# Kernel optimization log

Measured on AMD Instinct MI355X. Metric: run time of the kernel, lower is better.

## Reference

```python
import jax, jax.numpy as jnp
import numpy as np

ALPHA = 0.1   # margin alpha from __init__
K = 16        # retrieval fan-out
N_CLASSES = 100  # label range for mode computation (vals in [-1, N_CLASSES))


def setup_inputs() -> dict:
    key = jax.random.key(0)
    k1, k2, k3, k4 = jax.random.split(key, 4)
    queries = jax.random.normal(k1, (64, 512, 7, 7), dtype=jnp.float32)
    targets = jax.random.randint(k2, (64,), 0, 100, dtype=jnp.int32)
    m_keys = jax.random.normal(k3, (65536, 512), dtype=jnp.float32)
    m_keys = m_keys / jnp.linalg.norm(m_keys, axis=-1, keepdims=True)
    m_vals = jax.random.randint(k4, (65536,), 0, 100, dtype=jnp.int32)
    return {"queries": queries, "targets": targets, "m_keys": m_keys, "m_vals": m_vals}


def _forward(queries, targets, m_keys, m_vals):
    bs, c, h, w = queries.shape
    hw = h * w
    q = queries.reshape(bs, c, hw).transpose(0, 2, 1)            # [bs, hw, c]
    q = q / jnp.clip(jnp.linalg.norm(q, axis=-1, keepdims=True), 1e-12)  # F.normalize

    def per_item(qry, tgt):
        sims = qry @ m_keys.T                                    # [hw, M]
        # top-2 retrieval: fetched value = mode of nearest slot labels
        _, top2_idx = jax.lax.top_k(sims, 2)
        nearest_val = m_vals[top2_idx[:, 0]]                     # [hw]
        counts = jnp.zeros((N_CLASSES + 1,), jnp.int32).at[nearest_val + 1].add(1)
        fetched = jnp.argmax(counts).astype(jnp.int32) - 1
        # top-K retrieval for margin loss
        topk_sims, topk_idx = jax.lax.top_k(sims, K)             # [hw, K]
        topk_vals = m_vals[topk_idx]                             # [hw, K]
        # safety positive slot: first memory slot whose label == target
        hit = m_vals == tgt
        exists = jnp.any(hit)
        safety_idx = jnp.argmax(hit)
        safety_sim = sims[:, safety_idx]                         # [hw]
        ext_sims = jnp.concatenate([topk_sims, safety_sim[:, None]], axis=1)  # [hw, K+1]
        ext_vals = jnp.concatenate(
            [topk_vals, jnp.full((hw, 1), tgt, topk_vals.dtype)], axis=1)
        cmask = ext_vals == tgt
        pos = jnp.max(ext_sims * cmask, axis=-1)                 # topk(sims*mask, k=1)
        neg = jnp.max(ext_sims * (~cmask), axis=-1)
        loss_with = jnp.mean(jax.nn.relu(neg - pos + ALPHA))
        # branch where target class absent from memory
        neg_ns = jnp.max(topk_sims * (topk_vals != tgt), axis=-1)
        loss_ns = jnp.mean(jax.nn.relu(neg_ns + ALPHA))
        loss = jnp.where(exists, loss_with, loss_ns)
        return fetched, loss

    fetched_vals, losses = jax.vmap(per_item)(q, targets)
    return fetched_vals, jnp.sum(losses)


def reference(queries, targets, m_keys, m_vals):
    return _forward(queries, targets, m_keys, m_vals)
```

## Files before the change

### kernel.cpp

```cpp
#include <hip/hip_runtime.h>
#include <hip/hip_bf16.h>
#include <float.h>
#include <limits.h>

#define NROWS 3136
#define NROWS_PAD 3200
#define NKEYS 65536
#define KDIM 512
#define NITEMS 64
#define HW 49
#define TOPK 16
#define CAND 32
#define LANE_L 12
#define TKW 4
#define ALPHA_C 0.1f

typedef unsigned short u16;
typedef unsigned int u32;
typedef __attribute__((ext_vector_type(8))) short bfrag;
typedef __attribute__((ext_vector_type(4))) float f32x4;

__device__ inline u16 f2bf(float x) {
  u32 u = __float_as_uint(x);
  u32 r = u + 0x7fffu + ((u >> 16) & 1u);
  return (u16)(r >> 16);
}

__global__ __launch_bounds__(256) void prep_qnorm(const float* __restrict__ q,
        float* __restrict__ q_norm, u16* __restrict__ qbf) {
  int row = blockIdx.x;
  int t = threadIdx.x;
  if (row >= NROWS) {
    qbf[(size_t)row * KDIM + t] = 0;
    qbf[(size_t)row * KDIM + t + 256] = 0;
    return;
  }
  int b = row / HW, p = row % HW;
  const float* base = q + (size_t)b * KDIM * HW + p;
  float v0 = base[(size_t)t * HW];
  float v1 = base[(size_t)(t + 256) * HW];
  __shared__ float red[256];
  red[t] = v0 * v0 + v1 * v1;
  __syncthreads();
  for (int st = 128; st > 0; st >>= 1) {
    if (t < st) red[t] += red[t + st];
    __syncthreads();
  }
  float nrm = fmaxf(sqrtf(red[0]), 1e-12f);
  float w0 = v0 / nrm, w1 = v1 / nrm;
  q_norm[(size_t)row * KDIM + t] = w0;
  q_norm[(size_t)row * KDIM + t + 256] = w1;
  qbf[(size_t)row * KDIM + t] = f2bf(w0);
  qbf[(size_t)row * KDIM + t + 256] = f2bf(w1);
}

__global__ __launch_bounds__(256) void prep_keys(const float* __restrict__ mk, u16* __restrict__ kbf) {
  size_t i = ((size_t)blockIdx.x * 256 + threadIdx.x) * 8;
  float4 a = *(const float4*)(mk + i);
  float4 b = *(const float4*)(mk + i + 4);
  bfrag v;
  v[0] = (short)f2bf(a.x); v[1] = (short)f2bf(a.y);
  v[2] = (short)f2bf(a.z); v[3] = (short)f2bf(a.w);
  v[4] = (short)f2bf(b.x); v[5] = (short)f2bf(b.y);
  v[6] = (short)f2bf(b.z); v[7] = (short)f2bf(b.w);
  *(bfrag*)(kbf + i) = v;
}

__global__ void init_first(int* first_idx) {
  int t = threadIdx.x;
  if (t < 100) first_idx[t] = INT_MAX;
}
__global__ __launch_bounds__(256) void init_run(float* run_sim, int* run_idx) {
  int i = blockIdx.x * 256 + threadIdx.x;
  run_sim[i] = -FLT_MAX;
  run_idx[i] = INT_MAX;
}
__global__ __launch_bounds__(256) void scan_vals(const int* __restrict__ mvals, int* first_idx) {
  int i = blockIdx.x * 256 + threadIdx.x;
  atomicMin(&first_idx[mvals[i]], i);
}
__global__ void item_info(const int* __restrict__ targets, const int* __restrict__ first_idx,
                          int* item_saf, int* item_ex) {
  int b = threadIdx.x;
  int fi = first_idx[targets[b]];
  int ex = (fi != INT_MAX);
  item_ex[b] = ex;
  item_saf[b] = ex ? fi : 0;
}

__device__ inline void gload16(const void* g, void* l) {
  __builtin_amdgcn_global_load_lds((const __attribute__((address_space(1))) unsigned int*)g,
                                   (__attribute__((address_space(3))) unsigned int*)l, 16, 0, 0);
}

#define CT_LD 144

__global__ __launch_bounds__(256) void gemm_chunk(const u16* __restrict__ A, const u16* __restrict__ B,
        u16* __restrict__ C, int ldc) {
  __shared__ __align__(16) char lds[128 * CT_LD * 2];
  u16* As = (u16*)lds;
  u16* Bs = (u16*)(lds + 8192);
  u16* Ct = (u16*)lds;
  int tid = threadIdx.x;
  int lane = tid & 63, wv = tid >> 6;
  int wr = wv >> 1, wc = wv & 1;
  int mbase = blockIdx.x * 128;
  int nbase = blockIdx.y * 128;
  const u16* Ag = A + (size_t)mbase * KDIM;
  const u16* Bg = B + (size_t)nbase * KDIM;

  f32x4 acc[4][4];
  #pragma unroll
  for (int i = 0; i < 4; ++i)
    #pragma unroll
    for (int j = 0; j < 4; ++j)
      acc[i][j] = (f32x4){0.f, 0.f, 0.f, 0.f};

  int lrow = lane & 15;
  int k8 = (lane >> 4) * 8;

  for (int kk = 0; kk < KDIM; kk += 32) {
    #pragma unroll
    for (int s = 0; s < 2; ++s) {
      int ch = s * 256 + wv * 64 + lane;
      int r = ch >> 2, c = (ch & 3) * 8;
      gload16(Ag + (size_t)r * KDIM + kk + c, lds + (size_t)(s * 256 + wv * 64) * 16);
      gload16(Bg + (size_t)r * KDIM + kk + c, lds + 8192 + (size_t)(s * 256 + wv * 64) * 16);
    }
    __syncthreads();
    bfrag a[4], b[4];
    #pragma unroll
    for (int i = 0; i < 4; ++i) {
      a[i] = *(const bfrag*)&As[(wr * 64 + i * 16 + lrow) * 32 + k8];
      b[i] = *(const bfrag*)&Bs[(wc * 64 + i * 16 + lrow) * 32 + k8];
    }
    #pragma unroll
    for (int i = 0; i < 4; ++i)
      #pragma unroll
      for (int j = 0; j < 4; ++j)
        acc[i][j] = __builtin_amdgcn_mfma_f32_16x16x32_bf16(a[i], b[j], acc[i][j], 0, 0, 0);
    __syncthreads();
  }
  int r0l = wr * 64 + (lane >> 4) * 4;
  int c0l = wc * 64 + lrow;
  #pragma unroll
  for (int i = 0; i < 4; ++i)
    #pragma unroll
    for (int j = 0; j < 4; ++j)
      #pragma unroll
      for (int r = 0; r < 4; ++r)
        Ct[(r0l + i * 16 + r) * CT_LD + c0l + j * 16] = f2bf(acc[i][j][r]);
  __syncthreads();
  #pragma unroll
  for (int it = 0; it < 8; ++it) {
    int chnk = it * 256 + tid;
    int rr = chnk >> 4, cg = chnk & 15;
    uint4 v = *(const uint4*)&Ct[rr * CT_LD + cg * 8];
    *(uint4*)(C + (size_t)(mbase + rr) * ldc + nbase + cg * 8) = v;
  }
}

__device__ inline void ins_top(float (&s)[LANE_L], int (&ix)[LANE_L], float vv, int cidx) {
  if (vv > s[LANE_L - 1]) {
    #pragma unroll
    for (int k = LANE_L - 1; k >= 0; --k) {
      bool g  = vv > s[k];
      bool gp = (k > 0) && (vv > s[k - 1]);
      float ns = g ? (gp ? s[k - 1] : vv) : s[k];
      int   ni = g ? (gp ? ix[k - 1] : cidx) : ix[k];
      s[k] = ns; ix[k] = ni;
    }
  }
}

__global__ __launch_bounds__(256) void topk_update(const u16* __restrict__ C, int nk, int key_base,
        float* __restrict__ run_sim, int* __restrict__ run_idx) {
  int row = blockIdx.x;
  int tid = threadIdx.x, lane = tid & 63, wv = tid >> 6;
  int seg = nk >> 2;
  const u16* crow = C + (size_t)row * nk + (size_t)wv * seg;
  int ibase = key_base + wv * seg;

  float s[LANE_L]; int ix[LANE_L];
  #pragma unroll
  for (int k = 0; k < LANE_L; ++k) { s[k] = -FLT_MAX; ix[k] = INT_MAX; }

  int iters = seg >> 9;
  for (int t = 0; t < iters; ++t) {
    uint4 v = *(const uint4*)(crow + (size_t)t * 512 + lane * 8);
    int ib = ibase + t * 512 + lane * 8;
    ins_top(s, ix, __uint_as_float(v.x << 16), ib + 0);
    ins_top(s, ix, __uint_as_float(v.x & 0xffff0000u), ib + 1);
    ins_top(s, ix, __uint_as_float(v.y << 16), ib + 2);
    ins_top(s, ix, __uint_as_float(v.y & 0xffff0000u), ib + 3);
    ins_top(s, ix, __uint_as_float(v.z << 16), ib + 4);
    ins_top(s, ix, __uint_as_float(v.z & 0xffff0000u), ib + 5);
    ins_top(s, ix, __uint_as_float(v.w << 16), ib + 6);
    ins_top(s, ix, __uint_as_float(v.w & 0xffff0000u), ib + 7);
  }

  __shared__ float msim[TKW][CAND + 1]; __shared__ int midx[TKW][CAND + 1];
  __shared__ float rs[CAND + 1];        __shared__ int ri[CAND + 1];
  for (int r = 0; r < CAND; ++r) {
    float c = s[0]; int ci = ix[0];
    for (int off = 32; off > 0; off >>= 1) {
      float oc = __shfl_xor(c, off);
      int   oi = __shfl_xor(ci, off);
      if (oc > c || (oc == c && oi < ci)) { c = oc; ci = oi; }
    }
    if (lane == 0) { msim[wv][r] = c; midx[wv][r] = ci; }
    if (ci == ix[0]) {
      #pragma unroll
      for (int k = 0; k < LANE_L - 1; ++k) { s[k] = s[k + 1]; ix[k] = ix[k + 1]; }
      s[LANE_L - 1] = -FLT_MAX; ix[LANE_L - 1] = INT_MAX;
    }
  }
  if (lane == 0) { msim[wv][CAND] = -FLT_MAX; midx[wv][CAND] = INT_MAX; }
  if (tid < CAND) { rs[tid] = run_sim[row * CAND + tid]; ri[tid] = run_idx[row * CAND + tid]; }
  if (tid == 0)  { rs[CAND] = -FLT_MAX; ri[CAND] = INT_MAX; }
  __syncthreads();
  if (tid == 0) {
    int p0 = 0, p1 = 0, p2 = 0, p3 = 0, pr = 0;
    for (int o = 0; o < CAND; ++o) {
      float bs = rs[pr]; int bi = ri[pr]; int src = 4;
      float h; int hi;
      h = msim[0][p0]; hi = midx[0][p0]; if (h > bs || (h == bs && hi < bi)) { bs = h; bi = hi; src = 0; }
      h = msim[1][p1]; hi = midx[1][p1]; if (h > bs || (h == bs && hi < bi)) { bs = h; bi = hi; src = 1; }
      h = msim[2][p2]; hi = midx[2][p2]; if (h > bs || (h == bs && hi < bi)) { bs = h; bi = hi; src = 2; }
      h = msim[3][p3]; hi = midx[3][p3]; if (h > bs || (h == bs && hi < bi)) { bs = h; bi = hi; src = 3; }
      run_sim[row * CAND + o] = bs; run_idx[row * CAND + o] = bi;
      if (src == 0) ++p0; else if (src == 1) ++p1; else if (src == 2) ++p2;
      else if (src == 3) ++p3; else ++pr;
    }
  }
}

__global__ __launch_bounds__(64) void rescore(const float* __restrict__ q_norm, const float* __restrict__ mkeys,
        const int* __restrict__ mvals, const int* __restrict__ run_idx, const int* __restrict__ item_saf,
        float* __restrict__ t16_sim, int* __restrict__ t16_val, int* __restrict__ nearest_val,
        float* __restrict__ safety_sim) {
  int row = blockIdx.x, lane = threadIdx.x;
  int b = row / HW;
  const float* qr = q_norm + (size_t)row * KDIM;
  float4 q0 = *(const float4*)(qr + lane * 8);
  float4 q1 = *(const float4*)(qr + lane * 8 + 4);
  __shared__ float es[CAND]; __shared__ int ei[CAND];

  for (int c = 0; c < CAND; ++c) {
    int ki = run_idx[row * CAND + c];
    float p = -FLT_MAX;
    if (ki >= 0 && ki < NKEYS) {
      const float* kr = mkeys + (size_t)ki * KDIM;
      float4 k0 = *(const float4*)(kr + lane * 8);
      float4 k1 = *(const float4*)(kr + lane * 8 + 4);
      p = q0.x * k0.x + q0.y * k0.y + q0.z * k0.z + q0.w * k0.w
        + q1.x * k1.x + q1.y * k1.y + q1.z * k1.z + q1.w * k1.w;
      for (int off = 32; off > 0; off >>= 1) p += __shfl_xor(p, off);
    }
    if (lane == 0) { es[c] = p; ei[c] = (ki >= 0 && ki < NKEYS) ? ki : -1; }
  }
  {
    int ks = item_saf[b];
    const float* kr = mkeys + (size_t)ks * KDIM;
    float4 k0 = *(const float4*)(kr + lane * 8);
    float4 k1 = *(const float4*)(kr + lane * 8 + 4);
    float p = q0.x * k0.x + q0.y * k0.y + q0.z * k0.z + q0.w * k0.w
            + q1.x * k1.x + q1.y * k1.y + q1.z * k1.z + q1.w * k1.w;
    for (int off = 32; off > 0; off >>= 1) p += __shfl_xor(p, off);
    if (lane == 0) safety_sim[row] = p;
  }
  __syncthreads();
  if (lane == 0) {
    for (int r = 0; r < TOPK; ++r) {
      float bs = -FLT_MAX; int bi = INT_MAX, bc = -1;
      for (int c = 0; c < CAND; ++c) {
        if (ei[c] < 0) continue;
        if (es[c] > bs || (es[c] == bs && ei[c] < bi)) { bs = es[c]; bi = ei[c]; bc = c; }
      }
      if (bc < 0) { bs = 0.f; bi = 0; } else ei[bc] = -1;
      t16_sim[row * TOPK + r] = bs;
      t16_val[row * TOPK + r] = mvals[bi];
      if (r == 0) nearest_val[row] = mvals[bi];
    }
  }
}

__global__ __launch_bounds__(64) void item_loss(const float* __restrict__ t16_sim, const int* __restrict__ t16_val,
        const int* __restrict__ nearest_val, const float* __restrict__ safety_sim,
        const int* __restrict__ targets, const int* __restrict__ item_ex,
        float* __restrict__ losses, float* __restrict__ out) {
  int b = blockIdx.x, lane = threadIdx.x;
  __shared__ int counts[101];
  counts[lane] = 0;
  if (lane + 64 < 101) counts[lane + 64] = 0;
  __syncthreads();
  float lw = 0.f, lns = 0.f;
  if (lane < HW) {
    int row = b * HW + lane;
    int tgt = targets[b];
    float pos = -FLT_MAX, neg = -FLT_MAX, ns = -FLT_MAX;
    for (int k = 0; k < TOPK; ++k) {
      float sv = t16_sim[row * TOPK + k];
      int vv = t16_val[row * TOPK + k];
      bool m = (vv == tgt);
      pos = fmaxf(pos, m ? sv : 0.0f);
      neg = fmaxf(neg, m ? 0.0f : sv);
      ns  = fmaxf(ns,  m ? 0.0f : sv);
    }
    pos = fmaxf(pos, safety_sim[row]);
    neg = fmaxf(neg, 0.0f);
    lw  = fmaxf(neg - pos + ALPHA_C, 0.0f);
    lns = fmaxf(ns + ALPHA_C, 0.0f);
    atomicAdd(&counts[nearest_val[row] + 1], 1);
  }
  __syncthreads();
  for (int off = 32; off > 0; off >>= 1) {
    lw  += __shfl_xor(lw, off);
    lns += __shfl_xor(lns, off);
  }
  if (lane == 0) {
    int bi = 0, bc = counts[0];
    for (int c = 1; c < 101; ++c)
      if (counts[c] > bc) { bc = counts[c]; bi = c; }
    out[b] = (float)(bi - 1);
    losses[b] = (item_ex[b] ? lw : lns) / 49.0f;
  }
}

__global__ __launch_bounds__(64) void final_sum(const float* __restrict__ losses, float* __restrict__ out) {
  int lane = threadIdx.x;
  float v = losses[lane];
  for (int off = 32; off > 0; off >>= 1) v += __shfl_xor(v, off);
  if (lane == 0) out[NITEMS] = v;
}

extern "C" void kernel_launch(void* const* d_in, const int* in_sizes, int n_in,
                              void* d_out, int out_size, void* d_ws, size_t ws_size,
                              hipStream_t stream) {
  const float* queries = (const float*)d_in[0];
  const int*   targets = (const int*)d_in[1];
  const float* m_keys  = (const float*)d_in[2];
  const int*   m_vals  = (const int*)d_in[3];
  float* out = (float*)d_out;
  char* ws = (char*)d_ws;

  size_t off = 0;
  auto alloc = [&](size_t bytes) -> char* {
    char* p = ws + off;
    off += (bytes + 255) & ~(size_t)255;
    return p;
  };
  float* q_norm   = (float*)alloc((size_t)NROWS * KDIM * 4);
  u16*   qbf      = (u16*)  alloc((size_t)NROWS_PAD * KDIM * 2);
  u16*   kbf      = (u16*)  alloc((size_t)NKEYS * KDIM * 2);
  int*   first_ix = (int*)  alloc(128 * 4);
  int*   item_saf = (int*)  alloc(64 * 4);
  int*   item_ex  = (int*)  alloc(64 * 4);
  float* run_sim  = (float*)alloc((size_t)NROWS * CAND * 4);
  int*   run_idx  = (int*)  alloc((size_t)NROWS * CAND * 4);
  float* t16s     = (float*)alloc((size_t)NROWS * TOPK * 4);
  int*   t16v     = (int*)  alloc((size_t)NROWS * TOPK * 4);
  int*   nearv    = (int*)  alloc((size_t)NROWS * 4);
  float* safs     = (float*)alloc((size_t)NROWS * 4);
  float* losses   = (float*)alloc(64 * 4);
  u16*   sims     = (u16*)(ws + off);

  size_t avail = ws_size > off ? ws_size - off : 0;
  long long maxkeys = (long long)(avail / ((size_t)NROWS_PAD * 2));
  int chunk = (int)((maxkeys / 2048) * 2048);
  if (chunk > NKEYS) chunk = NKEYS;
  if (chunk < 2048) chunk = 2048;

  hipLaunchKernelGGL(prep_qnorm, dim3(NROWS_PAD), dim3(256), 0, stream, queries, q_norm, qbf);
  hipLaunchKernelGGL(prep_keys, dim3((NKEYS * KDIM) / 2048), dim3(256), 0, stream, m_keys, kbf);
  hipLaunchKernelGGL(init_first, dim3(1), dim3(128), 0, stream, first_ix);
  hipLaunchKernelGGL(init_run, dim3((NROWS * CAND) / 256), dim3(256), 0, stream, run_sim, run_idx);
  hipLaunchKernelGGL(scan_vals, dim3(NKEYS / 256), dim3(256), 0, stream, m_vals, first_ix);
  hipLaunchKernelGGL(item_info, dim3(1), dim3(64), 0, stream, targets, first_ix, item_saf, item_ex);

  for (int base = 0; base < NKEYS; base += chunk) {
    int nk = (NKEYS - base < chunk) ? (NKEYS - base) : chunk;
    hipLaunchKernelGGL(gemm_chunk, dim3(NROWS_PAD / 128, nk / 128), dim3(256), 0, stream,
                       qbf, kbf + (size_t)base * KDIM, sims, nk);
    hipLaunchKernelGGL(topk_update, dim3(NROWS), dim3(256), 0, stream, sims, nk, base, run_sim, run_idx);
  }

  hipLaunchKernelGGL(rescore, dim3(NROWS), dim3(64), 0, stream,
                     q_norm, m_keys, m_vals, run_idx, item_saf, t16s, t16v, nearv, safs);
  hipLaunchKernelGGL(item_loss, dim3(64), dim3(64), 0, stream,
                     t16s, t16v, nearv, safs, targets, item_ex, losses, out);
  hipLaunchKernelGGL(final_sum, dim3(1), dim3(64), 0, stream, losses, out);
}
```

Before: 1.211 ms.

## Replace per-lane insertion top-k with threshold filter and shared-buffer selection

The per-lane sorted insertion top-k is replaced by a two-pass scheme. The first pass computes per-thread maxima and derives a threshold as the 32nd-largest of those maxima. The second pass appends elements at or above the threshold into a shared buffer via atomics, and one wave then selects the top 32 merged with the running list. This avoids branchy per-element insertion work, but reads the chunk twice and can silently drop candidates if more than 1024 pass the threshold. The chunk size is also capped at 16384 keys, which changes the number of GEMM/top-k iterations.

```diff
diff --git a/kernel.cpp b/kernel.cpp
--- a/kernel.cpp
+++ b/kernel.cpp
@@ -11,8 +11,8 @@
 #define HW 49
 #define TOPK 16
 #define CAND 32
-#define LANE_L 12
-#define TKW 4
+#define TCAP 1024
+#define CHUNK_MAX 16384
 #define ALPHA_C 0.1f
 
 typedef unsigned short u16;
@@ -160,20 +160,7 @@
   }
 }
 
-__device__ inline void ins_top(float (&s)[LANE_L], int (&ix)[LANE_L], float vv, int cidx) {
-  if (vv > s[LANE_L - 1]) {
-    #pragma unroll
-    for (int k = LANE_L - 1; k >= 0; --k) {
-      bool g  = vv > s[k];
-      bool gp = (k > 0) && (vv > s[k - 1]);
-      float ns = g ? (gp ? s[k - 1] : vv) : s[k];
-      int   ni = g ? (gp ? ix[k - 1] : cidx) : ix[k];
-      s[k] = ns; ix[k] = ni;
-    }
-  }
-}
-
-__global__ __launch_bounds__(256) void topk_update(const u16* __restrict__ C, int nk, int key_base,
+__global__ __launch_bounds__(256) void topk_select(const u16* __restrict__ C, int nk, int key_base,
         float* __restrict__ run_sim, int* __restrict__ run_idx) {
   int row = blockIdx.x;
   int tid = threadIdx.x, lane = tid & 63, wv = tid >> 6;
@@ -181,56 +168,108 @@
   const u16* crow = C + (size_t)row * nk + (size_t)wv * seg;
   int ibase = key_base + wv * seg;
 
-  float s[LANE_L]; int ix[LANE_L];
+  __shared__ float lmax[256];
+  __shared__ float Tsh;
+  __shared__ int cnt;
+  __shared__ float bval[TCAP];
+  __shared__ int bidx[TCAP];
+
   #pragma unroll
-  for (int k = 0; k < LANE_L; ++k) { s[k] = -FLT_MAX; ix[k] = INT_MAX; }
-
+  for (int k = 0; k < TCAP / 256; ++k) { bval[tid + k * 256] = -FLT_MAX; bidx[tid + k * 256] = INT_MAX; }
+  if (tid == 0) cnt = 0;
+
+  float pm = -FLT_MAX;
   int iters = seg >> 9;
   for (int t = 0; t < iters; ++t) {
     uint4 v = *(const uint4*)(crow + (size_t)t * 512 + lane * 8);
-    int ib = ibase + t * 512 + lane * 8;
-    ins_top(s, ix, __uint_as_float(v.x << 16), ib + 0);
-    ins_top(s, ix, __uint_as_float(v.x & 0xffff0000u), ib + 1);
-    ins_top(s, ix, __uint_as_float(v.y << 16), ib + 2);
-    ins_top(s, ix, __uint_as_float(v.y & 0xffff0000u), ib + 3);
-    ins_top(s, ix, __uint_as_float(v.z << 16), ib + 4);
-    ins_top(s, ix, __uint_as_float(v.z & 0xffff0000u), ib + 5);
-    ins_top(s, ix, __uint_as_float(v.w << 16), ib + 6);
-    ins_top(s, ix, __uint_as_float(v.w & 0xffff0000u), ib + 7);
-  }
-
-  __shared__ float msim[TKW][CAND + 1]; __shared__ int midx[TKW][CAND + 1];
-  __shared__ float rs[CAND + 1];        __shared__ int ri[CAND + 1];
-  for (int r = 0; r < CAND; ++r) {
-    float c = s[0]; int ci = ix[0];
-    for (int off = 32; off > 0; off >>= 1) {
-      float oc = __shfl_xor(c, off);
-      int   oi = __shfl_xor(ci, off);
-      if (oc > c || (oc == c && oi < ci)) { c = oc; ci = oi; }
-    }
-    if (lane == 0) { msim[wv][r] = c; midx[wv][r] = ci; }
-    if (ci == ix[0]) {
+    pm = fmaxf(pm, __uint_as_float(v.x << 16));
+    pm = fmaxf(pm, __uint_as_float(v.x & 0xffff0000u));
+    pm = fmaxf(pm, __uint_as_float(v.y << 16));
+    pm = fmaxf(pm, __uint_as_float(v.y & 0xffff0000u));
+    pm = fmaxf(pm, __uint_as_float(v.z << 16));
+    pm = fmaxf(pm, __uint_as_float(v.z & 0xffff0000u));
+    pm = fmaxf(pm, __uint_as_float(v.w << 16));
+    pm = fmaxf(pm, __uint_as_float(v.w & 0xffff0000u));
+  }
+  lmax[tid] = pm;
+  __syncthreads();
+
+  if (wv == 0) {
+    float v0 = lmax[lane * 4 + 0];
+    float v1 = lmax[lane * 4 + 1];
+    float v2 = lmax[lane * 4 + 2];
+    float v3 = lmax[lane * 4 + 3];
+    float T = 0.f;
+    for (int r = 0; r < CAND; ++r) {
+      float lm = fmaxf(fmaxf(v0, v1), fmaxf(v2, v3));
+      float wm = lm;
+      for (int off = 32; off > 0; off >>= 1) wm = fmaxf(wm, __shfl_xor(wm, off));
+      if (lm == wm) {
+        if      (v0 == wm) v0 = -FLT_MAX;
+        else if (v1 == wm) v1 = -FLT_MAX;
+        else if (v2 == wm) v2 = -FLT_MAX;
+        else               v3 = -FLT_MAX;
+      }
+      T = wm;
+    }
+    if (lane == 0) Tsh = T;
+  }
+  __syncthreads();
+  float T = Tsh;
+
+  for (int t = 0; t < iters; ++t) {
+    uint4 v = *(const uint4*)(crow + (size_t)t * 512 + lane * 8);
+    float f0 = __uint_as_float(v.x << 16);
+    float f1 = __uint_as_float(v.x & 0xffff0000u);
+    float f2 = __uint_as_float(v.y << 16);
+    float f3 = __uint_as_float(v.y & 0xffff0000u);
+    float f4 = __uint_as_float(v.z << 16);
+    float f5 = __uint_as_float(v.z & 0xffff0000u);
+    float f6 = __uint_as_float(v.w << 16);
+    float f7 = __uint_as_float(v.w & 0xffff0000u);
+    float m8 = fmaxf(fmaxf(fmaxf(f0, f1), fmaxf(f2, f3)),
+                     fmaxf(fmaxf(f4, f5), fmaxf(f6, f7)));
+    if (m8 >= T) {
+      int ib = ibase + t * 512 + lane * 8;
+      if (f0 >= T) { int p = atomicAdd(&cnt, 1); if (p < TCAP) { bval[p] = f0; bidx[p] = ib + 0; } }
+      if (f1 >= T) { int p = atomicAdd(&cnt, 1); if (p < TCAP) { bval[p] = f1; bidx[p] = ib + 1; } }
+      if (f2 >= T) { int p = atomicAdd(&cnt, 1); if (p < TCAP) { bval[p] = f2; bidx[p] = ib + 2; } }
+      if (f3 >= T) { int p = atomicAdd(&cnt, 1); if (p < TCAP) { bval[p] = f3; bidx[p] = ib + 3; } }
+      if (f4 >= T) { int p = atomicAdd(&cnt, 1); if (p < TCAP) { bval[p] = f4; bidx[p] = ib + 4; } }
+      if (f5 >= T) { int p = atomicAdd(&cnt, 1); if (p < TCAP) { bval[p] = f5; bidx[p] = ib + 5; } }
+      if (f6 >= T) { int p = atomicAdd(&cnt, 1); if (p < TCAP) { bval[p] = f6; bidx[p] = ib + 6; } }
+      if (f7 >= T) { int p = atomicAdd(&cnt, 1); if (p < TCAP) { bval[p] = f7; bidx[p] = ib + 7; } }
+    }
+  }
+  __syncthreads();
+  if (wv == 0 && lane < CAND) {
+    int p = atomicAdd(&cnt, 1);
+    if (p < TCAP) { bval[p] = run_sim[row * CAND + lane]; bidx[p] = run_idx[row * CAND + lane]; }
+  }
+  __syncthreads();
+
+  if (wv == 0) {
+    float sv[16]; int si[16];
+    #pragma unroll
+    for (int k = 0; k < 16; ++k) { sv[k] = bval[lane * 16 + k]; si[k] = bidx[lane * 16 + k]; }
+    for (int r = 0; r < CAND; ++r) {
+      float lm = -FLT_MAX; int li = INT_MAX;
       #pragma unroll
-      for (int k = 0; k < LANE_L - 1; ++k) { s[k] = s[k + 1]; ix[k] = ix[k + 1]; }
-      s[LANE_L - 1] = -FLT_MAX; ix[LANE_L - 1] = INT_MAX;
-    }
-  }
-  if (lane == 0) { msim[wv][CAND] = -FLT_MAX; midx[wv][CAND] = INT_MAX; }
-  if (tid < CAND) { rs[tid] = run_sim[row * CAND + tid]; ri[tid] = run_idx[row * CAND + tid]; }
-  if (tid == 0)  { rs[CAND] = -FLT_MAX; ri[CAND] = INT_MAX; }
-  __syncthreads();
-  if (tid == 0) {
-    int p0 = 0, p1 = 0, p2 = 0, p3 = 0, pr = 0;
-    for (int o = 0; o < CAND; ++o) {
-      float bs = rs[pr]; int bi = ri[pr]; int src = 4;
-      float h; int hi;
-      h = msim[0][p0]; hi = midx[0][p0]; if (h > bs || (h == bs && hi < bi)) { bs = h; bi = hi; src = 0; }
-      h = msim[1][p1]; hi = midx[1][p1]; if (h > bs || (h == bs && hi < bi)) { bs = h; bi = hi; src = 1; }
-      h = msim[2][p2]; hi = midx[2][p2]; if (h > bs || (h == bs && hi < bi)) { bs = h; bi = hi; src = 2; }
-      h = msim[3][p3]; hi = midx[3][p3]; if (h > bs || (h == bs && hi < bi)) { bs = h; bi = hi; src = 3; }
-      run_sim[row * CAND + o] = bs; run_idx[row * CAND + o] = bi;
-      if (src == 0) ++p0; else if (src == 1) ++p1; else if (src == 2) ++p2;
-      else if (src == 3) ++p3; else ++pr;
+      for (int k = 0; k < 16; ++k)
+        if (sv[k] > lm || (sv[k] == lm && si[k] < li)) { lm = sv[k]; li = si[k]; }
+      float plm = lm; int pli = li;
+      for (int off = 32; off > 0; off >>= 1) {
+        float ov = __shfl_xor(lm, off);
+        int   oi = __shfl_xor(li, off);
+        if (ov > lm || (ov == lm && oi < li)) { lm = ov; li = oi; }
+      }
+      if (lane == 0) { run_sim[row * CAND + r] = lm; run_idx[row * CAND + r] = li; }
+      if (plm == lm && pli == li) {
+        bool done = false;
+        #pragma unroll
+        for (int k = 0; k < 16; ++k)
+          if (!done && sv[k] == lm && si[k] == li) { sv[k] = -FLT_MAX; si[k] = INT_MAX; done = true; }
+      }
     }
   }
 }
@@ -368,7 +407,7 @@
   size_t avail = ws_size > off ? ws_size - off : 0;
   long long maxkeys = (long long)(avail / ((size_t)NROWS_PAD * 2));
   int chunk = (int)((maxkeys / 2048) * 2048);
-  if (chunk > NKEYS) chunk = NKEYS;
+  if (chunk > CHUNK_MAX) chunk = CHUNK_MAX;
   if (chunk < 2048) chunk = 2048;
 
   hipLaunchKernelGGL(prep_qnorm, dim3(NROWS_PAD), dim3(256), 0, stream, queries, q_norm, qbf);
@@ -382,7 +421,7 @@
     int nk = (NKEYS - base < chunk) ? (NKEYS - base) : chunk;
     hipLaunchKernelGGL(gemm_chunk, dim3(NROWS_PAD / 128, nk / 128), dim3(256), 0, stream,
                        qbf, kbf + (size_t)base * KDIM, sims, nk);
-    hipLaunchKernelGGL(topk_update, dim3(NROWS), dim3(256), 0, stream, sims, nk, base, run_sim, run_idx);
+    hipLaunchKernelGGL(topk_select, dim3(NROWS), dim3(256), 0, stream, sims, nk, base, run_sim, run_idx);
   }
 
   hipLaunchKernelGGL(rescore, dim3(NROWS), dim3(64), 0, stream,
```

Result: slower. 1.294 ms (+6.8%).
